# Kernel tuning notes

Measured on AMD Instinct MI355X. Metric: run time of the kernel, lower is better.

## Reference

```python
import jax, jax.numpy as jnp
import numpy as np

B, N, D, H, C = 2048, 6, 2048, 1024, 200  # batch, nodes/graph, feat dim, hidden, classes
ALPHA = 0.015   # distance decay in edge weight
SCALE = 24.0    # weight rescale after mean-subtraction + clamp


def setup_inputs() -> dict:
    key = jax.random.key(0)
    k1, k2, k3, k4 = jax.random.split(key, 4)
    part_feats = jax.random.normal(k1, (B, N, D), dtype=jnp.float32)
    # cdds columns: [score, y0, x0, y1, x1, idx]; only cols 1:5 (box coords) are used
    cdds = jax.random.uniform(k2, (B, N, 6), dtype=jnp.float32) * 448.0
    fc_w = jax.random.normal(k3, (2 * D, H), dtype=jnp.float32) * 0.02
    fc_b = jnp.zeros((H,), dtype=jnp.float32)
    cls_w = jax.random.normal(k4, (H, C), dtype=jnp.float32) * 0.02
    cls_b = jnp.zeros((C,), dtype=jnp.float32)
    return {"part_feats": part_feats, "cdds": cdds, "fc_w": fc_w, "fc_b": fc_b,
            "cls_w": cls_w, "cls_b": cls_b}


def reference(part_feats, cdds, fc_w, fc_b, cls_w, cls_b):
    # --- edge weights on per-sample complete graph (apply_edges) ---
    loc = cdds[:, :, 1:5]                      # (B, N, 4) = (y0, x0, y1, x1)
    cy = (loc[..., 0] + loc[..., 2]) * 0.5     # node center y, (B, N)
    cx = (loc[..., 1] + loc[..., 3]) * 0.5     # node center x, (B, N)
    dx = cx[:, :, None] - cx[:, None, :]       # (B, N, N) pairwise
    dy = cy[:, :, None] - cy[:, None, :]
    d2 = dx * dx + dy * dy
    mask = ~jnp.eye(N, dtype=bool)             # off-diagonal = real edges (30 per graph)
    dist = jnp.sqrt(jnp.where(mask, d2, 1.0))  # safe sqrt off the diagonal
    w0 = jnp.where(mask, jnp.exp(-ALPHA * dist), 0.0)
    mean_w = jnp.sum(w0, axis=(1, 2), keepdims=True) / (N * (N - 1))  # mean over 30 edges
    w = SCALE * jnp.maximum(w0 - mean_w, 0.0) * mask                  # (B, N, N), w[b,u,v]
    # --- update_all: u_mul_e + mean over the (N-1) incoming edges per node ---
    hidden = jnp.einsum('buv,bud->bvd', w, part_feats) / (N - 1)      # (B, N, D)
    # --- node MLP + graph mean readout + classifier ---
    node_ft = jnp.concatenate([hidden, part_feats], axis=-1) @ fc_w + fc_b  # (B, N, H)
    g_ft = node_ft.mean(axis=1)                                             # (B, H)
    return g_ft @ cls_w + cls_b                                             # (B, C)
```

## Files before the change

### kernel.cpp

```cpp
#include <hip/hip_runtime.h>
#include <math.h>

namespace {
constexpr int NB = 2048;
constexpr int NNODE = 6;
constexpr int DD = 2048;
constexpr int HH = 1024;
constexpr int CC = 200;
constexpr int K2 = 2 * DD;
constexpr int NPAD = 256;
constexpr int ZS1 = 4;
constexpr int ZS2 = 16;
constexpr float ALPHA_C = 0.015f;
constexpr float SCALE_C = 24.0f;

constexpr int G1_BLOCKS = (K2 / 32) * ZS1;
constexpr int PQ_BLOCKS = 1024;
}

typedef __attribute__((ext_vector_type(8))) short bf16x8;
typedef __attribute__((ext_vector_type(4))) float f32x4;

static __device__ __forceinline__ unsigned short f2bf(float x) {
    union { float f; unsigned int u; } v; v.f = x;
    unsigned int r = v.u + 0x7FFFu + ((v.u >> 16) & 1u);
    return (unsigned short)(r >> 16);
}

static __device__ __forceinline__ float bf2f(unsigned short u) {
    union { unsigned int i; float f; } v; v.i = ((unsigned int)u) << 16;
    return v.f;
}

static __device__ __forceinline__ unsigned pack2(float a, float b) {
    return (unsigned)f2bf(a) | ((unsigned)f2bf(b) << 16);
}

static __device__ __forceinline__ float compute_s_lane(const float* __restrict__ cdds,
                                                       int b, int* u_out) {
    const int lane = threadIdx.x & 63;
    const int u = lane >> 3;
    const int v = lane & 7;
    *u_out = u;
    const float* cd = cdds + (size_t)b * 36;
    float w = 0.f;
    const bool valid = (u < 6) & (v < 6) & (u != v);
    if (u < 6 && v < 6 && u != v) {
        float cyu = (cd[u * 6 + 1] + cd[u * 6 + 3]) * 0.5f;
        float cxu = (cd[u * 6 + 2] + cd[u * 6 + 4]) * 0.5f;
        float cyv = (cd[v * 6 + 1] + cd[v * 6 + 3]) * 0.5f;
        float cxv = (cd[v * 6 + 2] + cd[v * 6 + 4]) * 0.5f;
        float dx = cxu - cxv, dy = cyu - cyv;
        w = expf(-ALPHA_C * sqrtf(dx * dx + dy * dy));
    }
    float s = w;
#pragma unroll
    for (int m = 32; m >= 1; m >>= 1) s += __shfl_xor(s, m);
    float mean = s * (1.f / 30.f);
    float tt = valid ? fmaxf(w - mean, 0.f) : 0.f;
    tt += __shfl_xor(tt, 1);
    tt += __shfl_xor(tt, 2);
    tt += __shfl_xor(tt, 4);
    return SCALE_C * tt * 0.2f;
}

__global__ __launch_bounds__(256) void k_small(const float* __restrict__ cls_w,
                                               const float* __restrict__ fc_b,
                                               const float* __restrict__ cls_b,
                                               const float* __restrict__ cdds,
                                               unsigned short* __restrict__ cls_wT,
                                               float* __restrict__ bvec,
                                               float* __restrict__ sbuf)
{
    __shared__ float sm[64 * 65];
    const int bx = blockIdx.x;
    const int t = threadIdx.x;
    if (bx >= 89) {
        const int b = (bx - 89) * 4 + (t >> 6);
        int u;
        float su = compute_s_lane(cdds, b, &u);
        if ((t & 7) == 0 && u < 6) sbuf[b * 6 + u] = su;
        return;
    }
    if (bx >= 64) {
        const int bb = bx - 64;
        float* red = sm;
        int c8 = t & 7;
        int hs = t >> 3;
        int c = bb * 8 + c8;
        float acc = 0.f;
        for (int h = hs; h < HH; h += 32)
            acc += fc_b[h] * cls_w[(size_t)h * CC + c];
        red[t] = acc;
        __syncthreads();
        for (int s = 128; s >= 8; s >>= 1) {
            if (t < s) red[t] += red[t + s];
            __syncthreads();
        }
        if (t < 8) bvec[c] = red[t] + cls_b[c];
        return;
    }
    const int kt = bx & 15;
    const int nt = bx >> 4;
#pragma unroll
    for (int c = 0; c < 4; ++c) {
        int i = t + c * 256;
        int kr = i >> 4;
        int n4 = (i & 15) << 2;
        int gn = nt * 64 + n4;
        const float* sp = cls_w + (size_t)(kt * 64 + kr) * CC + gn;
        float4 v = {0.f, 0.f, 0.f, 0.f};
        if (gn + 3 < CC) {
            v = *(const float4*)sp;
        } else {
            if (gn + 0 < CC) v.x = sp[0];
            if (gn + 1 < CC) v.y = sp[1];
            if (gn + 2 < CC) v.z = sp[2];
            if (gn + 3 < CC) v.w = sp[3];
        }
        sm[kr * 65 + n4 + 0] = v.x; sm[kr * 65 + n4 + 1] = v.y;
        sm[kr * 65 + n4 + 2] = v.z; sm[kr * 65 + n4 + 3] = v.w;
    }
    __syncthreads();
#pragma unroll
    for (int c = 0; c < 4; ++c) {
        int i = t + c * 256;
        int nr = i >> 4;
        int k4 = (i & 15) << 2;
        ushort4 o;
        o.x = f2bf(sm[(k4 + 0) * 65 + nr]);
        o.y = f2bf(sm[(k4 + 1) * 65 + nr]);
        o.z = f2bf(sm[(k4 + 2) * 65 + nr]);
        o.w = f2bf(sm[(k4 + 3) * 65 + nr]);
        *(ushort4*)(cls_wT + (size_t)(nt * 64 + nr) * HH + kt * 64 + k4) = o;
    }
}

__global__ __launch_bounds__(256) void k_mid(const float* __restrict__ pf,
                                             const float* __restrict__ sbuf,
                                             const float* __restrict__ fc_w,
                                             const unsigned short* __restrict__ Bt,
                                             unsigned short* __restrict__ pq,
                                             float* __restrict__ partM)
{
    __shared__ short As[32][72];
    __shared__ short Bs[256][72];
    const int bx = blockIdx.x;
    const int t = threadIdx.x;

    if (bx >= G1_BLOCKS) {
        const int d = t << 3;
        for (int b = bx - G1_BLOCKS; b < NB; b += PQ_BLOCKS) {
            const float* base = pf + (size_t)b * NNODE * DD + d;
            float4 a00 = *(const float4*)(base + 0 * DD);
            float4 a01 = *(const float4*)(base + 0 * DD + 4);
            float4 a10 = *(const float4*)(base + 1 * DD);
            float4 a11 = *(const float4*)(base + 1 * DD + 4);
            float4 a20 = *(const float4*)(base + 2 * DD);
            float4 a21 = *(const float4*)(base + 2 * DD + 4);
            float4 a30 = *(const float4*)(base + 3 * DD);
            float4 a31 = *(const float4*)(base + 3 * DD + 4);
            float4 a40 = *(const float4*)(base + 4 * DD);
            float4 a41 = *(const float4*)(base + 4 * DD + 4);
            float4 a50 = *(const float4*)(base + 5 * DD);
            float4 a51 = *(const float4*)(base + 5 * DD + 4);
            float s0 = sbuf[b * 6 + 0], s1 = sbuf[b * 6 + 1];
            float s2 = sbuf[b * 6 + 2], s3 = sbuf[b * 6 + 3];
            float s4 = sbuf[b * 6 + 4], s5 = sbuf[b * 6 + 5];

            float4 q0, q1, p0 = {0, 0, 0, 0}, p1 = {0, 0, 0, 0};
            q0.x = a00.x + a10.x + a20.x + a30.x + a40.x + a50.x;
            q0.y = a00.y + a10.y + a20.y + a30.y + a40.y + a50.y;
            q0.z = a00.z + a10.z + a20.z + a30.z + a40.z + a50.z;
            q0.w = a00.w + a10.w + a20.w + a30.w + a40.w + a50.w;
            q1.x = a01.x + a11.x + a21.x + a31.x + a41.x + a51.x;
            q1.y = a01.y + a11.y + a21.y + a31.y + a41.y + a51.y;
            q1.z = a01.z + a11.z + a21.z + a31.z + a41.z + a51.z;
            q1.w = a01.w + a11.w + a21.w + a31.w + a41.w + a51.w;

            p0.x = fmaf(s0, a00.x, p0.x); p0.y = fmaf(s0, a00.y, p0.y);
            p0.z = fmaf(s0, a00.z, p0.z); p0.w = fmaf(s0, a00.w, p0.w);
            p1.x = fmaf(s0, a01.x, p1.x); p1.y = fmaf(s0, a01.y, p1.y);
            p1.z = fmaf(s0, a01.z, p1.z); p1.w = fmaf(s0, a01.w, p1.w);
            p0.x = fmaf(s1, a10.x, p0.x); p0.y = fmaf(s1, a10.y, p0.y);
            p0.z = fmaf(s1, a10.z, p0.z); p0.w = fmaf(s1, a10.w, p0.w);
            p1.x = fmaf(s1, a11.x, p1.x); p1.y = fmaf(s1, a11.y, p1.y);
            p1.z = fmaf(s1, a11.z, p1.z); p1.w = fmaf(s1, a11.w, p1.w);
            p0.x = fmaf(s2, a20.x, p0.x); p0.y = fmaf(s2, a20.y, p0.y);
            p0.z = fmaf(s2, a20.z, p0.z); p0.w = fmaf(s2, a20.w, p0.w);
            p1.x = fmaf(s2, a21.x, p1.x); p1.y = fmaf(s2, a21.y, p1.y);
            p1.z = fmaf(s2, a21.z, p1.z); p1.w = fmaf(s2, a21.w, p1.w);
            p0.x = fmaf(s3, a30.x, p0.x); p0.y = fmaf(s3, a30.y, p0.y);
            p0.z = fmaf(s3, a30.z, p0.z); p0.w = fmaf(s3, a30.w, p0.w);
            p1.x = fmaf(s3, a31.x, p1.x); p1.y = fmaf(s3, a31.y, p1.y);
            p1.z = fmaf(s3, a31.z, p1.z); p1.w = fmaf(s3, a31.w, p1.w);
            p0.x = fmaf(s4, a40.x, p0.x); p0.y = fmaf(s4, a40.y, p0.y);
            p0.z = fmaf(s4, a40.z, p0.z); p0.w = fmaf(s4, a40.w, p0.w);
            p1.x = fmaf(s4, a41.x, p1.x); p1.y = fmaf(s4, a41.y, p1.y);
            p1.z = fmaf(s4, a41.z, p1.z); p1.w = fmaf(s4, a41.w, p1.w);
            p0.x = fmaf(s5, a50.x, p0.x); p0.y = fmaf(s5, a50.y, p0.y);
            p0.z = fmaf(s5, a50.z, p0.z); p0.w = fmaf(s5, a50.w, p0.w);
            p1.x = fmaf(s5, a51.x, p1.x); p1.y = fmaf(s5, a51.y, p1.y);
            p1.z = fmaf(s5, a51.z, p1.z); p1.w = fmaf(s5, a51.w, p1.w);

            unsigned short* o = pq + (size_t)b * K2;
            uint4 po, qo;
            po.x = pack2(p0.x, p0.y); po.y = pack2(p0.z, p0.w);
            po.z = pack2(p1.x, p1.y); po.w = pack2(p1.z, p1.w);
            qo.x = pack2(q0.x, q0.y); qo.y = pack2(q0.z, q0.w);
            qo.z = pack2(q1.x, q1.y); qo.w = pack2(q1.z, q1.w);
            *(uint4*)(o + d) = po;
            *(uint4*)(o + DD + d) = qo;
        }
        return;
    }

    const int lane = t & 63;
    const int wid = t >> 6;
    const int bm = (bx >> 2) * 32;
    const int z = bx & 3;
    const int kbase = z * (HH / ZS1);

    f32x4 acc[2][4] = {};

    for (int k0 = kbase; k0 < kbase + HH / ZS1; k0 += 64) {
#pragma unroll
        for (int c = 0; c < 2; ++c) {
            int i = t + c * 256;
            int row = i >> 4;
            int k4 = (i & 15) << 2;
            float4 v = *(const float4*)(fc_w + (size_t)(bm + row) * HH + k0 + k4);
            ushort4 o;
            o.x = f2bf(v.x); o.y = f2bf(v.y); o.z = f2bf(v.z); o.w = f2bf(v.w);
            *(ushort4*)&As[row][k4] = o;
        }
#pragma unroll
        for (int c = 0; c < 8; ++c) {
            int i = t + c * 256;
            int n = i >> 3;
            int k8 = (i & 7) << 3;
            *(uint4*)&Bs[n][k8] =
                *(const uint4*)(Bt + (size_t)n * HH + k0 + k8);
        }
        __syncthreads();
#pragma unroll
        for (int ks = 0; ks < 2; ++ks) {
            int kk = ks * 32 + ((lane >> 4) << 3);
            int ar = lane & 15;
            bf16x8 a0 = *(const bf16x8*)&As[ar][kk];
            bf16x8 a1 = *(const bf16x8*)&As[16 + ar][kk];
#pragma unroll
            for (int fn = 0; fn < 4; ++fn) {
                bf16x8 b = *(const bf16x8*)&Bs[wid * 64 + fn * 16 + ar][kk];
                acc[0][fn] = __builtin_amdgcn_mfma_f32_16x16x32_bf16(a0, b, acc[0][fn], 0, 0, 0);
                acc[1][fn] = __builtin_amdgcn_mfma_f32_16x16x32_bf16(a1, b, acc[1][fn], 0, 0, 0);
            }
        }
        __syncthreads();
    }
#pragma unroll
    for (int fm = 0; fm < 2; ++fm)
#pragma unroll
        for (int fn = 0; fn < 4; ++fn) {
            int gm0 = bm + fm * 16 + ((lane >> 4) << 2);
            int gn = wid * 64 + fn * 16 + (lane & 15);
#pragma unroll
            for (int r = 0; r < 4; ++r)
                partM[((size_t)z * K2 + gm0 + r) * NPAD + gn] = acc[fm][fn][r];
        }
}

__global__ __launch_bounds__(256) void k_red(const float* __restrict__ partM,
                                             unsigned short* __restrict__ Mt)
{
    __shared__ float sm[64][69];
    const int bx = blockIdx.x;
    const int t = threadIdx.x;
    const int bm = (bx >> 2) * 64;
    const int bn = (bx & 3) * 64;
#pragma unroll
    for (int c = 0; c < 4; ++c) {
        int i = t + c * 256;
        int mr = i >> 4;
        int n4 = (i & 15) << 2;
        float4 s = {0.f, 0.f, 0.f, 0.f};
#pragma unroll
        for (int z = 0; z < ZS1; ++z) {
            float4 v = *(const float4*)(partM +
                ((size_t)z * K2 + bm + mr) * NPAD + bn + n4);
            s.x += v.x; s.y += v.y; s.z += v.z; s.w += v.w;
        }
        sm[mr][n4 + 0] = s.x; sm[mr][n4 + 1] = s.y;
        sm[mr][n4 + 2] = s.z; sm[mr][n4 + 3] = s.w;
    }
    __syncthreads();
#pragma unroll
    for (int c = 0; c < 4; ++c) {
        int i = t + c * 256;
        int nr = i >> 4;
        int m4 = (i & 15) << 2;
        ushort4 o;
        o.x = f2bf(sm[m4 + 0][nr]);
        o.y = f2bf(sm[m4 + 1][nr]);
        o.z = f2bf(sm[m4 + 2][nr]);
        o.w = f2bf(sm[m4 + 3][nr]);
        *(ushort4*)(Mt + (size_t)(bn + nr) * K2 + bm + m4) = o;
    }
}

__global__ __launch_bounds__(256) void k_gemm2(const unsigned short* __restrict__ A,
                                               const unsigned short* __restrict__ Bt,
                                               unsigned short* __restrict__ part)
{
    __shared__ short As[64][72];
    __shared__ short Bs[256][72];
    const int t = threadIdx.x;
    const int lane = t & 63;
    const int wid = t >> 6;
    const int bm = blockIdx.x * 64;
    const int z = blockIdx.y;
    const int kbase = z * (K2 / ZS2);

    f32x4 acc[4][4] = {};

    for (int k0 = kbase; k0 < kbase + K2 / ZS2; k0 += 64) {
#pragma unroll
        for (int c = 0; c < 2; ++c) {
            int i = t + c * 256;
            int row = i >> 3;
            int k8 = (i & 7) << 3;
            *(uint4*)&As[row][k8] =
                *(const uint4*)(A + (size_t)(bm + row) * K2 + k0 + k8);
        }
#pragma unroll
        for (int c = 0; c < 8; ++c) {
            int i = t + c * 256;
            int n = i >> 3;
            int k8 = (i & 7) << 3;
            *(uint4*)&Bs[n][k8] =
                *(const uint4*)(Bt + (size_t)n * K2 + k0 + k8);
        }
        __syncthreads();
#pragma unroll
        for (int ks = 0; ks < 2; ++ks) {
            int kk = ks * 32 + ((lane >> 4) << 3);
            int ar = lane & 15;
            bf16x8 a0 = *(const bf16x8*)&As[0 * 16 + ar][kk];
            bf16x8 a1 = *(const bf16x8*)&As[1 * 16 + ar][kk];
            bf16x8 a2 = *(const bf16x8*)&As[2 * 16 + ar][kk];
            bf16x8 a3 = *(const bf16x8*)&As[3 * 16 + ar][kk];
#pragma unroll
            for (int fn = 0; fn < 4; ++fn) {
                bf16x8 b = *(const bf16x8*)&Bs[wid * 64 + fn * 16 + ar][kk];
                acc[0][fn] = __builtin_amdgcn_mfma_f32_16x16x32_bf16(a0, b, acc[0][fn], 0, 0, 0);
                acc[1][fn] = __builtin_amdgcn_mfma_f32_16x16x32_bf16(a1, b, acc[1][fn], 0, 0, 0);
                acc[2][fn] = __builtin_amdgcn_mfma_f32_16x16x32_bf16(a2, b, acc[2][fn], 0, 0, 0);
                acc[3][fn] = __builtin_amdgcn_mfma_f32_16x16x32_bf16(a3, b, acc[3][fn], 0, 0, 0);
            }
        }
        __syncthreads();
    }
#pragma unroll
    for (int fm = 0; fm < 4; ++fm)
#pragma unroll
        for (int fn = 0; fn < 4; ++fn) {
            int gm0 = bm + fm * 16 + ((lane >> 4) << 2);
            int gn = wid * 64 + fn * 16 + (lane & 15);
#pragma unroll
            for (int r = 0; r < 4; ++r)
                part[((size_t)z * NB + gm0 + r) * NPAD + gn] = f2bf(acc[fm][fn][r]);
        }
}

__global__ __launch_bounds__(256) void k_combine(const unsigned short* __restrict__ part,
                                                 const float* __restrict__ bvec,
                                                 float* __restrict__ out)
{
    int idx = blockIdx.x * blockDim.x + threadIdx.x;
    if (idx >= NB * (CC / 4)) return;
    int b = idx / (CC / 4);
    int c0 = (idx - b * (CC / 4)) << 2;
    float s0 = 0.f, s1 = 0.f, s2 = 0.f, s3 = 0.f;
#pragma unroll
    for (int z = 0; z < ZS2; ++z) {
        ushort4 v = *(const ushort4*)(part + ((size_t)z * NB + b) * NPAD + c0);
        s0 += bf2f(v.x); s1 += bf2f(v.y); s2 += bf2f(v.z); s3 += bf2f(v.w);
    }
    float4 o;
    o.x = s0 * (1.f / 6.f) + bvec[c0 + 0];
    o.y = s1 * (1.f / 6.f) + bvec[c0 + 1];
    o.z = s2 * (1.f / 6.f) + bvec[c0 + 2];
    o.w = s3 * (1.f / 6.f) + bvec[c0 + 3];
    *(float4*)(out + (size_t)b * CC + c0) = o;
}

extern "C" void kernel_launch(void* const* d_in, const int* in_sizes, int n_in,
                              void* d_out, int out_size, void* d_ws, size_t ws_size,
                              hipStream_t stream)
{
    const float* part_feats = (const float*)d_in[0];
    const float* cdds = (const float*)d_in[1];
    const float* fc_w = (const float*)d_in[2];
    const float* fc_b = (const float*)d_in[3];
    const float* cls_w = (const float*)d_in[4];
    const float* cls_b = (const float*)d_in[5];
    float* out = (float*)d_out;

    char* ws = (char*)d_ws;
    size_t off = 0;
    unsigned short* pq = (unsigned short*)(ws + off);     off += (size_t)NB * K2 * 2;
    unsigned short* Mt = (unsigned short*)(ws + off);     off += (size_t)NPAD * K2 * 2;
    unsigned short* cls_wT = (unsigned short*)(ws + off); off += (size_t)NPAD * HH * 2;
    float* partM = (float*)(ws + off);                    off += (size_t)ZS1 * K2 * NPAD * 4;
    unsigned short* part = (unsigned short*)(ws + off);   off += (size_t)ZS2 * NB * NPAD * 2;
    float* bvec = (float*)(ws + off);                     off += 256 * 4;
    float* sbuf = (float*)(ws + off);                     off += (size_t)NB * NNODE * 4;

    k_small<<<dim3(64 + 25 + NB / 4), dim3(256), 0, stream>>>(
        cls_w, fc_b, cls_b, cdds, cls_wT, bvec, sbuf);
    k_mid<<<dim3(G1_BLOCKS + PQ_BLOCKS), dim3(256), 0, stream>>>(
        part_feats, sbuf, fc_w, cls_wT, pq, partM);
    k_red<<<dim3(256), dim3(256), 0, stream>>>(partM, Mt);
    k_gemm2<<<dim3(NB / 64, ZS2), dim3(256), 0, stream>>>(pq, Mt, part);
    k_combine<<<dim3((NB * (CC / 4) + 255) / 256), dim3(256), 0, stream>>>(part, bvec, out);
}
```

Baseline: 73.17 us.

## Split fused mid kernel into separate GEMM and pq kernels with software-pipelined loads

Splits the combined k_mid kernel, which ran the fc_w×cls_wT GEMM blocks and the per-graph p/q reduction blocks side by side, into two separate launches. The new pq kernel handles 4 graphs per block and issues the next graph's row loads before computing the current one, keeping more memory requests in flight. The split gives up the concurrency of both workloads sharing one grid and adds an extra launch, trading it for simpler, specialised blocks. The pq kernel also declares launch bounds of (256, 1).

Result: no change. 73.09 us (-0.1%).

```diff
diff --git a/kernel.cpp b/kernel.cpp
--- a/kernel.cpp
+++ b/kernel.cpp
@@ -13,9 +13,6 @@
 constexpr int ZS2 = 16;
 constexpr float ALPHA_C = 0.015f;
 constexpr float SCALE_C = 24.0f;
-
-constexpr int G1_BLOCKS = (K2 / 32) * ZS1;
-constexpr int PQ_BLOCKS = 1024;
 }
 
 typedef __attribute__((ext_vector_type(8))) short bf16x8;
@@ -136,89 +133,17 @@
     }
 }
 
-__global__ __launch_bounds__(256) void k_mid(const float* __restrict__ pf,
-                                             const float* __restrict__ sbuf,
-                                             const float* __restrict__ fc_w,
-                                             const unsigned short* __restrict__ Bt,
-                                             unsigned short* __restrict__ pq,
-                                             float* __restrict__ partM)
+__global__ __launch_bounds__(256) void k_g1(const float* __restrict__ fc_w,
+                                            const unsigned short* __restrict__ Bt,
+                                            float* __restrict__ partM)
 {
     __shared__ short As[32][72];
     __shared__ short Bs[256][72];
-    const int bx = blockIdx.x;
     const int t = threadIdx.x;
-
-    if (bx >= G1_BLOCKS) {
-        const int d = t << 3;
-        for (int b = bx - G1_BLOCKS; b < NB; b += PQ_BLOCKS) {
-            const float* base = pf + (size_t)b * NNODE * DD + d;
-            float4 a00 = *(const float4*)(base + 0 * DD);
-            float4 a01 = *(const float4*)(base + 0 * DD + 4);
-            float4 a10 = *(const float4*)(base + 1 * DD);
-            float4 a11 = *(const float4*)(base + 1 * DD + 4);
-            float4 a20 = *(const float4*)(base + 2 * DD);
-            float4 a21 = *(const float4*)(base + 2 * DD + 4);
-            float4 a30 = *(const float4*)(base + 3 * DD);
-            float4 a31 = *(const float4*)(base + 3 * DD + 4);
-            float4 a40 = *(const float4*)(base + 4 * DD);
-            float4 a41 = *(const float4*)(base + 4 * DD + 4);
-            float4 a50 = *(const float4*)(base + 5 * DD);
-            float4 a51 = *(const float4*)(base + 5 * DD + 4);
-            float s0 = sbuf[b * 6 + 0], s1 = sbuf[b * 6 + 1];
-            float s2 = sbuf[b * 6 + 2], s3 = sbuf[b * 6 + 3];
-            float s4 = sbuf[b * 6 + 4], s5 = sbuf[b * 6 + 5];
-
-            float4 q0, q1, p0 = {0, 0, 0, 0}, p1 = {0, 0, 0, 0};
-            q0.x = a00.x + a10.x + a20.x + a30.x + a40.x + a50.x;
-            q0.y = a00.y + a10.y + a20.y + a30.y + a40.y + a50.y;
-            q0.z = a00.z + a10.z + a20.z + a30.z + a40.z + a50.z;
-            q0.w = a00.w + a10.w + a20.w + a30.w + a40.w + a50.w;
-            q1.x = a01.x + a11.x + a21.x + a31.x + a41.x + a51.x;
-            q1.y = a01.y + a11.y + a21.y + a31.y + a41.y + a51.y;
-            q1.z = a01.z + a11.z + a21.z + a31.z + a41.z + a51.z;
-            q1.w = a01.w + a11.w + a21.w + a31.w + a41.w + a51.w;
-
-            p0.x = fmaf(s0, a00.x, p0.x); p0.y = fmaf(s0, a00.y, p0.y);
-            p0.z = fmaf(s0, a00.z, p0.z); p0.w = fmaf(s0, a00.w, p0.w);
-            p1.x = fmaf(s0, a01.x, p1.x); p1.y = fmaf(s0, a01.y, p1.y);
-            p1.z = fmaf(s0, a01.z, p1.z); p1.w = fmaf(s0, a01.w, p1.w);
-            p0.x = fmaf(s1, a10.x, p0.x); p0.y = fmaf(s1, a10.y, p0.y);
-            p0.z = fmaf(s1, a10.z, p0.z); p0.w = fmaf(s1, a10.w, p0.w);
-            p1.x = fmaf(s1, a11.x, p1.x); p1.y = fmaf(s1, a11.y, p1.y);
-            p1.z = fmaf(s1, a11.z, p1.z); p1.w = fmaf(s1, a11.w, p1.w);
-            p0.x = fmaf(s2, a20.x, p0.x); p0.y = fmaf(s2, a20.y, p0.y);
-            p0.z = fmaf(s2, a20.z, p0.z); p0.w = fmaf(s2, a20.w, p0.w);
-            p1.x = fmaf(s2, a21.x, p1.x); p1.y = fmaf(s2, a21.y, p1.y);
-            p1.z = fmaf(s2, a21.z, p1.z); p1.w = fmaf(s2, a21.w, p1.w);
-            p0.x = fmaf(s3, a30.x, p0.x); p0.y = fmaf(s3, a30.y, p0.y);
-            p0.z = fmaf(s3, a30.z, p0.z); p0.w = fmaf(s3, a30.w, p0.w);
-            p1.x = fmaf(s3, a31.x, p1.x); p1.y = fmaf(s3, a31.y, p1.y);
-            p1.z = fmaf(s3, a31.z, p1.z); p1.w = fmaf(s3, a31.w, p1.w);
-            p0.x = fmaf(s4, a40.x, p0.x); p0.y = fmaf(s4, a40.y, p0.y);
-            p0.z = fmaf(s4, a40.z, p0.z); p0.w = fmaf(s4, a40.w, p0.w);
-            p1.x = fmaf(s4, a41.x, p1.x); p1.y = fmaf(s4, a41.y, p1.y);
-            p1.z = fmaf(s4, a41.z, p1.z); p1.w = fmaf(s4, a41.w, p1.w);
-            p0.x = fmaf(s5, a50.x, p0.x); p0.y = fmaf(s5, a50.y, p0.y);
-            p0.z = fmaf(s5, a50.z, p0.z); p0.w = fmaf(s5, a50.w, p0.w);
-            p1.x = fmaf(s5, a51.x, p1.x); p1.y = fmaf(s5, a51.y, p1.y);
-            p1.z = fmaf(s5, a51.z, p1.z); p1.w = fmaf(s5, a51.w, p1.w);
-
-            unsigned short* o = pq + (size_t)b * K2;
-            uint4 po, qo;
-            po.x = pack2(p0.x, p0.y); po.y = pack2(p0.z, p0.w);
-            po.z = pack2(p1.x, p1.y); po.w = pack2(p1.z, p1.w);
-            qo.x = pack2(q0.x, q0.y); qo.y = pack2(q0.z, q0.w);
-            qo.z = pack2(q1.x, q1.y); qo.w = pack2(q1.z, q1.w);
-            *(uint4*)(o + d) = po;
-            *(uint4*)(o + DD + d) = qo;
-        }
-        return;
-    }
-
     const int lane = t & 63;
     const int wid = t >> 6;
-    const int bm = (bx >> 2) * 32;
-    const int z = bx & 3;
+    const int bm = blockIdx.x * 32;
+    const int z = blockIdx.y;
     const int kbase = z * (HH / ZS1);
 
     f32x4 acc[2][4] = {};
@@ -268,6 +193,69 @@
             for (int r = 0; r < 4; ++r)
                 partM[((size_t)z * K2 + gm0 + r) * NPAD + gn] = acc[fm][fn][r];
         }
+}
+
+struct Rows { float4 r[12]; };
+
+static __device__ __forceinline__ Rows load_rows(const float* __restrict__ base) {
+    Rows x;
+#pragma unroll
+    for (int u = 0; u < NNODE; ++u) {
+        x.r[2 * u + 0] = *(const float4*)(base + (size_t)u * DD);
+        x.r[2 * u + 1] = *(const float4*)(base + (size_t)u * DD + 4);
+    }
+    return x;
+}
+
+static __device__ __forceinline__ void compute_store(const Rows& x,
+                                                     const float* __restrict__ sb,
+                                                     unsigned short* __restrict__ o,
+                                                     int d) {
+    float s0 = sb[0], s1 = sb[1], s2 = sb[2], s3 = sb[3], s4 = sb[4], s5 = sb[5];
+    float4 q0, q1, p0 = {0, 0, 0, 0}, p1 = {0, 0, 0, 0};
+    q0.x = x.r[0].x + x.r[2].x + x.r[4].x + x.r[6].x + x.r[8].x + x.r[10].x;
+    q0.y = x.r[0].y + x.r[2].y + x.r[4].y + x.r[6].y + x.r[8].y + x.r[10].y;
+    q0.z = x.r[0].z + x.r[2].z + x.r[4].z + x.r[6].z + x.r[8].z + x.r[10].z;
+    q0.w = x.r[0].w + x.r[2].w + x.r[4].w + x.r[6].w + x.r[8].w + x.r[10].w;
+    q1.x = x.r[1].x + x.r[3].x + x.r[5].x + x.r[7].x + x.r[9].x + x.r[11].x;
+    q1.y = x.r[1].y + x.r[3].y + x.r[5].y + x.r[7].y + x.r[9].y + x.r[11].y;
+    q1.z = x.r[1].z + x.r[3].z + x.r[5].z + x.r[7].z + x.r[9].z + x.r[11].z;
+    q1.w = x.r[1].w + x.r[3].w + x.r[5].w + x.r[7].w + x.r[9].w + x.r[11].w;
+    const float sv[6] = {s0, s1, s2, s3, s4, s5};
+#pragma unroll
+    for (int u = 0; u < 6; ++u) {
+        float s = sv[u];
+        p0.x = fmaf(s, x.r[2 * u].x, p0.x); p0.y = fmaf(s, x.r[2 * u].y, p0.y);
+        p0.z = fmaf(s, x.r[2 * u].z, p0.z); p0.w = fmaf(s, x.r[2 * u].w, p0.w);
+        p1.x = fmaf(s, x.r[2 * u + 1].x, p1.x); p1.y = fmaf(s, x.r[2 * u + 1].y, p1.y);
+        p1.z = fmaf(s, x.r[2 * u + 1].z, p1.z); p1.w = fmaf(s, x.r[2 * u + 1].w, p1.w);
+    }
+    uint4 po, qo;
+    po.x = pack2(p0.x, p0.y); po.y = pack2(p0.z, p0.w);
+    po.z = pack2(p1.x, p1.y); po.w = pack2(p1.z, p1.w);
+    qo.x = pack2(q0.x, q0.y); qo.y = pack2(q0.z, q0.w);
+    qo.z = pack2(q1.x, q1.y); qo.w = pack2(q1.z, q1.w);
+    *(uint4*)(o + d) = po;
+    *(uint4*)(o + DD + d) = qo;
+}
+
+__global__ __launch_bounds__(256, 1) void k_pq(const float* __restrict__ pf,
+                                               const float* __restrict__ sbuf,
+                                               unsigned short* __restrict__ pq)
+{
+    const int t = threadIdx.x;
+    const int d = t << 3;
+    const int b0 = blockIdx.x * 4;
+    const float* base = pf + (size_t)b0 * NNODE * DD + d;
+
+    Rows A = load_rows(base);
+    Rows B = load_rows(base + 1 * NNODE * DD);
+    compute_store(A, sbuf + (b0 + 0) * 6, pq + (size_t)(b0 + 0) * K2, d);
+    A = load_rows(base + 2 * NNODE * DD);
+    compute_store(B, sbuf + (b0 + 1) * 6, pq + (size_t)(b0 + 1) * K2, d);
+    B = load_rows(base + 3 * NNODE * DD);
+    compute_store(A, sbuf + (b0 + 2) * 6, pq + (size_t)(b0 + 2) * K2, d);
+    compute_store(B, sbuf + (b0 + 3) * 6, pq + (size_t)(b0 + 3) * K2, d);
 }
 
 __global__ __launch_bounds__(256) void k_red(const float* __restrict__ partM,
@@ -418,8 +406,8 @@
 
     k_small<<<dim3(64 + 25 + NB / 4), dim3(256), 0, stream>>>(
         cls_w, fc_b, cls_b, cdds, cls_wT, bvec, sbuf);
-    k_mid<<<dim3(G1_BLOCKS + PQ_BLOCKS), dim3(256), 0, stream>>>(
-        part_feats, sbuf, fc_w, cls_wT, pq, partM);
+    k_g1<<<dim3(K2 / 32, ZS1), dim3(256), 0, stream>>>(fc_w, cls_wT, partM);
+    k_pq<<<dim3(NB / 4), dim3(256), 0, stream>>>(part_feats, sbuf, pq);
     k_red<<<dim3(256), dim3(256), 0, stream>>>(partM, Mt);
     k_gemm2<<<dim3(NB / 64, ZS2), dim3(256), 0, stream>>>(pq, Mt, part);
     k_combine<<<dim3((NB * (CC / 4) + 255) / 256), dim3(256), 0, stream>>>(part, bvec, out);
```
